# Kernel optimization log

Hardware: AMD Instinct MI355X
Metric: run time of the kernel (lower is better)

The kernel has to match this reference:

```python
import jax, jax.numpy as jnp
import numpy as np

B = 64          # number of scenes/graphs
OBJS = 2048     # objects per scene
N = B * OBJS    # total objects
D = 256         # representation_dim
K = 2           # num_channels


def setup_inputs() -> dict:
    key = jax.random.key(0)
    k1, k2, k3 = jax.random.split(key, 3)
    x_aggregation = jax.random.normal(k1, (N, D), dtype=jnp.float32)
    num_objs = jnp.full((B,), OBJS, dtype=jnp.int32)
    # glorot for att_shared [1, D]: fan_in + fan_out = 1 + D
    std_shared = float(np.sqrt(6.0 / (1 + D)))
    att_shared = jax.random.uniform(k2, (1, D), dtype=jnp.float32,
                                    minval=-std_shared, maxval=std_shared)
    # glorot for att_scale [K, 1]
    std_scale = float(np.sqrt(6.0 / (K + 1)))
    att_scale = jax.random.uniform(k3, (K, 1), dtype=jnp.float32,
                                   minval=-std_scale, maxval=std_scale)
    channel_bias = jnp.zeros((K, D), dtype=jnp.float32)
    return {"x_aggregation": x_aggregation, "num_objs": num_objs,
            "att_shared": att_shared, "att_scale": att_scale,
            "channel_bias": channel_bias}


def reference(x_aggregation, num_objs, att_shared, att_scale, channel_bias):
    batch_idx = jnp.repeat(jnp.arange(B), num_objs, total_repeat_length=N)  # [N]
    # scatter_mean: per-scene context features [B, D]
    seg_sum = jax.ops.segment_sum(x_aggregation, batch_idx, num_segments=B)
    counts = jnp.maximum(num_objs, 1).astype(x_aggregation.dtype)
    ctx = seg_sum / counts[:, None]
    attn_in = jax.nn.leaky_relu(x_aggregation + ctx[batch_idx], negative_slope=0.2)  # [N, D]
    # per-channel logits: ((attn_in + bias[k]) . att_shared) * scale[k]
    base = attn_in @ att_shared[0]                 # [N]
    bias_term = channel_bias @ att_shared[0]       # [K]
    logits = (base[:, None] + bias_term[None, :]) * att_scale[:, 0][None, :]  # [N, K]
    # per-channel segment softmax over objects within each scene
    m = jax.ops.segment_max(logits, batch_idx, num_segments=B)   # [B, K]
    z = jnp.exp(logits - m[batch_idx])
    s = jax.ops.segment_sum(z, batch_idx, num_segments=B)        # [B, K]
    attn_weights = z / s[batch_idx]                              # [N, K]
    # attention-weighted pooling per channel -> [B, D, K]
    weighted = x_aggregation[:, :, None] * attn_weights[:, None, :]  # [N, D, K]
    scene_features = jax.ops.segment_sum(weighted, batch_idx, num_segments=B)
    return scene_features, attn_weights
```

## Files before the change

kernel.cpp:

```cpp
#include <hip/hip_runtime.h>

#define B    64
#define OBJS 2048
#define NTOT (B * OBJS)
#define D    256
#define K    2
#define S1   16
#define CH   (OBJS / S1)
#define RPW  (CH / 4)

#define WS_P1  0
#define WS_UP  (1024 * 256)
#define WS_ZP  (WS_UP + 1024 * 512)
#define WS_E   (WS_ZP + 1024 * 8)

static __device__ __forceinline__ float lrelu02(float v) {
    return v > 0.0f ? v : 0.2f * v;
}

__global__ __launch_bounds__(256) void k1_partial(const float* __restrict__ x,
                                                  float* __restrict__ ws) {
    __shared__ float red[4 * D];
    int blk = blockIdx.x;
    int w = threadIdx.x >> 6, l = threadIdx.x & 63;
    int row0 = blk * CH + w * RPW;

    float4 acc = make_float4(0.f, 0.f, 0.f, 0.f);
    const float* px = x + (size_t)row0 * D + 4 * l;
#pragma unroll 8
    for (int j = 0; j < RPW; ++j) {
        float4 v = *(const float4*)(px + (size_t)j * D);
        acc.x += v.x; acc.y += v.y; acc.z += v.z; acc.w += v.w;
    }
    *(float4*)(red + w * D + 4 * l) = acc;
    __syncthreads();
    int t = threadIdx.x;
    if (t < 64) {
        float4 a = ((const float4*)(red        ))[t];
        float4 e = ((const float4*)(red +     D))[t];
        float4 f = ((const float4*)(red + 2 * D))[t];
        float4 g = ((const float4*)(red + 3 * D))[t];
        float4 s = make_float4(a.x + e.x + f.x + g.x, a.y + e.y + f.y + g.y,
                               a.z + e.z + f.z + g.z, a.w + e.w + f.w + g.w);
        *(float4*)(ws + WS_P1 + blk * D + 4 * t) = s;
    }
}

__global__ __launch_bounds__(256) void k2_main(const float* __restrict__ x,
                                               const int* __restrict__ num_objs,
                                               const float* __restrict__ att_scale,
                                               const float* __restrict__ att_shared,
                                               const float* __restrict__ channel_bias,
                                               float* __restrict__ ws) {
    __shared__ float sctx[D];
    __shared__ float sbt[2];
    __shared__ float ured[4 * D * K];
    int blk = blockIdx.x;
    int b = blk >> 4;
    int t = threadIdx.x;
    int w = t >> 6, l = t & 63;
    int row0 = blk * CH + w * RPW;

    {
        int cnt = num_objs[b]; if (cnt < 1) cnt = 1;
        float inv = 1.0f / (float)cnt;
        float s = 0.f;
#pragma unroll
        for (int c = 0; c < S1; ++c) s += ws[WS_P1 + (b * S1 + c) * D + t];
        sctx[t] = s * inv;
    }
    if (t < 64) {
        float4 a = ((const float4*)att_shared)[t];
#pragma unroll
        for (int k = 0; k < K; ++k) {
            float4 cb = ((const float4*)(channel_bias + k * D))[t];
            float v = a.x * cb.x + a.y * cb.y + a.z * cb.z + a.w * cb.w;
#pragma unroll
            for (int m = 32; m > 0; m >>= 1) v += __shfl_xor(v, m);
            if (t == 0) sbt[k] = v;
        }
    }
    __syncthreads();

    float4 a4 = ((const float4*)att_shared)[l];
    float4 ctx4 = *(const float4*)(sctx + 4 * l);
    float bt0 = sbt[0], bt1 = sbt[1];
    float s0 = att_scale[0], s1 = att_scale[1];

    float4 acc0 = make_float4(0.f, 0.f, 0.f, 0.f);
    float4 acc1 = make_float4(0.f, 0.f, 0.f, 0.f);
    float z0 = 0.f, z1 = 0.f;
    float my_e0 = 0.f, my_e1 = 0.f;
    int sel = l & 31;
    const float* px = x + (size_t)row0 * D + 4 * l;

#pragma unroll 4
    for (int j = 0; j < RPW; ++j) {
        float4 v = *(const float4*)(px + (size_t)j * D);
        float p = lrelu02(v.x + ctx4.x) * a4.x
                + lrelu02(v.y + ctx4.y) * a4.y
                + lrelu02(v.z + ctx4.z) * a4.z
                + lrelu02(v.w + ctx4.w) * a4.w;
#pragma unroll
        for (int m = 32; m > 0; m >>= 1) p += __shfl_xor(p, m);
        float e0 = __expf((p + bt0) * s0);
        float e1 = __expf((p + bt1) * s1);
        z0 += e0; z1 += e1;
        acc0.x += v.x * e0; acc0.y += v.y * e0; acc0.z += v.z * e0; acc0.w += v.w * e0;
        acc1.x += v.x * e1; acc1.y += v.y * e1; acc1.z += v.z * e1; acc1.w += v.w * e1;
        if (j == sel) { my_e0 = e0; my_e1 = e1; }
    }

    if (l < 32) ((float2*)(ws + WS_E))[row0 + l] = make_float2(my_e0, my_e1);
    if (l == 0) {
        ws[WS_ZP + blk * 8 + w * 2 + 0] = z0;
        ws[WS_ZP + blk * 8 + w * 2 + 1] = z1;
    }
    int base = w * (D * K) + l * 8;
    ured[base + 0] = acc0.x; ured[base + 1] = acc1.x;
    ured[base + 2] = acc0.y; ured[base + 3] = acc1.y;
    ured[base + 4] = acc0.z; ured[base + 5] = acc1.z;
    ured[base + 6] = acc0.w; ured[base + 7] = acc1.w;
    __syncthreads();
    if (t < 128) {
        float4 a = ((const float4*)(ured       ))[t];
        float4 e = ((const float4*)(ured +  512))[t];
        float4 f = ((const float4*)(ured + 1024))[t];
        float4 g = ((const float4*)(ured + 1536))[t];
        float4 s = make_float4(a.x + e.x + f.x + g.x, a.y + e.y + f.y + g.y,
                               a.z + e.z + f.z + g.z, a.w + e.w + f.w + g.w);
        *(float4*)(ws + WS_UP + blk * (D * K) + 4 * t) = s;
    }
}

__global__ __launch_bounds__(256) void k3_final(const float* __restrict__ ws,
                                                float* __restrict__ out) {
    __shared__ float zsh[2];
    int b = blockIdx.x;
    int t = threadIdx.x;
    int w = t >> 6, l = t & 63;

    if (w < 2) {
        float v = ws[WS_ZP + (b * S1 + (l >> 2)) * 8 + (l & 3) * 2 + w];
#pragma unroll
        for (int m = 32; m > 0; m >>= 1) v += __shfl_xor(v, m);
        if (l == 0) zsh[w] = v;
    }
    __syncthreads();
    float z0 = zsh[0], z1 = zsh[1];

#pragma unroll
    for (int j = t; j < D * K; j += 256) {
        float s = 0.f;
#pragma unroll
        for (int c = 0; c < S1; ++c) s += ws[WS_UP + (b * S1 + c) * (D * K) + j];
        out[b * (D * K) + j] = s / ((j & 1) ? z1 : z0);
    }
    const float2* E = (const float2*)(ws + WS_E);
    float2* W = (float2*)(out + B * D * K);
#pragma unroll
    for (int i = t; i < OBJS; i += 256) {
        float2 e = E[b * OBJS + i];
        W[b * OBJS + i] = make_float2(e.x / z0, e.y / z1);
    }
}

extern "C" void kernel_launch(void* const* d_in, const int* in_sizes, int n_in,
                              void* d_out, int out_size, void* d_ws, size_t ws_size,
                              hipStream_t stream) {
    const float* x            = (const float*)d_in[0];
    const int*   num_objs     = (const int*)d_in[1];
    const float* att_shared   = (const float*)d_in[2];
    const float* att_scale    = (const float*)d_in[3];
    const float* channel_bias = (const float*)d_in[4];
    float* ws  = (float*)d_ws;
    float* out = (float*)d_out;

    k1_partial<<<B * S1, 256, 0, stream>>>(x, ws);
    k2_main<<<B * S1, 256, 0, stream>>>(x, num_objs, att_scale, att_shared,
                                        channel_bias, ws);
    k3_final<<<B, 256, 0, stream>>>(ws, out);
}
```

Measured before the change: 222.8 us.

## Fuse three kernels into one with per-scene spin barriers and register-cached rows

Merges the segment-sum, attention-pooling and finalize kernels into one launch that keeps each block's rows in registers and LDS. Scene-local atomic barriers replace the kernel boundaries, so x is read from global memory once instead of twice and the stored unnormalized exponentials disappear. The fused kernel relies on all 512 blocks being co-resident; if they are not, the spin barriers deadlock until the timeout breaks them. It also raises register and LDS pressure.

```diff
diff --git a/kernel.cpp b/kernel.cpp
--- a/kernel.cpp
+++ b/kernel.cpp
@@ -5,70 +5,97 @@
 #define NTOT (B * OBJS)
 #define D    256
 #define K    2
-#define S1   16
-#define CH   (OBJS / S1)
-#define RPW  (CH / 4)
+
+#define SPB   8
+#define GRID  (B * SPB)
+#define RPB   (OBJS / SPB)
+#define RPWV  (RPB / 4)
+#define NREG  45
+#define NLDS  19
 
 #define WS_P1  0
-#define WS_UP  (1024 * 256)
-#define WS_ZP  (WS_UP + 1024 * 512)
-#define WS_E   (WS_ZP + 1024 * 8)
+#define WS_UP  (GRID * 4 * 256)
+#define WS_ZP  (WS_UP + GRID * 512)
+#define WS_CNT (WS_ZP + GRID * 2)
 
 static __device__ __forceinline__ float lrelu02(float v) {
     return v > 0.0f ? v : 0.2f * v;
 }
 
-__global__ __launch_bounds__(256) void k1_partial(const float* __restrict__ x,
-                                                  float* __restrict__ ws) {
-    __shared__ float red[4 * D];
-    int blk = blockIdx.x;
-    int w = threadIdx.x >> 6, l = threadIdx.x & 63;
-    int row0 = blk * CH + w * RPW;
-
-    float4 acc = make_float4(0.f, 0.f, 0.f, 0.f);
-    const float* px = x + (size_t)row0 * D + 4 * l;
-#pragma unroll 8
-    for (int j = 0; j < RPW; ++j) {
-        float4 v = *(const float4*)(px + (size_t)j * D);
-        acc.x += v.x; acc.y += v.y; acc.z += v.z; acc.w += v.w;
-    }
-    *(float4*)(red + w * D + 4 * l) = acc;
-    __syncthreads();
-    int t = threadIdx.x;
-    if (t < 64) {
-        float4 a = ((const float4*)(red        ))[t];
-        float4 e = ((const float4*)(red +     D))[t];
-        float4 f = ((const float4*)(red + 2 * D))[t];
-        float4 g = ((const float4*)(red + 3 * D))[t];
-        float4 s = make_float4(a.x + e.x + f.x + g.x, a.y + e.y + f.y + g.y,
-                               a.z + e.z + f.z + g.z, a.w + e.w + f.w + g.w);
-        *(float4*)(ws + WS_P1 + blk * D + 4 * t) = s;
-    }
-}
-
-__global__ __launch_bounds__(256) void k2_main(const float* __restrict__ x,
-                                               const int* __restrict__ num_objs,
-                                               const float* __restrict__ att_scale,
-                                               const float* __restrict__ att_shared,
-                                               const float* __restrict__ channel_bias,
-                                               float* __restrict__ ws) {
+static __device__ __forceinline__ float ldg_agent(const float* p) {
+    return __hip_atomic_load(p, __ATOMIC_RELAXED, __HIP_MEMORY_SCOPE_AGENT);
+}
+
+static __device__ __forceinline__ void scene_barrier(int* cnt, int expect) {
+    __builtin_amdgcn_fence(__ATOMIC_RELEASE, "agent");
+    __syncthreads();
+    if (threadIdx.x == 0) {
+        __hip_atomic_fetch_add(cnt, 1, __ATOMIC_ACQ_REL, __HIP_MEMORY_SCOPE_AGENT);
+        int it = 0;
+        while (__hip_atomic_load(cnt, __ATOMIC_ACQUIRE, __HIP_MEMORY_SCOPE_AGENT) < expect) {
+            __builtin_amdgcn_s_sleep(2);
+            if (++it > (1 << 26)) break;
+        }
+    }
+    __syncthreads();
+    __builtin_amdgcn_fence(__ATOMIC_ACQUIRE, "agent");
+}
+
+#define ROW_BODY(JCONST, V)                                                   \
+    {                                                                         \
+        float p = lrelu02((V).x + ctx4.x) * a4.x                              \
+                + lrelu02((V).y + ctx4.y) * a4.y                              \
+                + lrelu02((V).z + ctx4.z) * a4.z                              \
+                + lrelu02((V).w + ctx4.w) * a4.w;                             \
+        _Pragma("unroll")                                                     \
+        for (int m_ = 32; m_ > 0; m_ >>= 1) p += __shfl_xor(p, m_);           \
+        float e0_ = __expf((p + bt0) * s0);                                   \
+        float e1_ = __expf((p + bt1) * s1);                                   \
+        if ((JCONST) == l) { e0c = e0_; e1c = e1_; }                          \
+        acc0.x += (V).x * e0_; acc0.y += (V).y * e0_;                         \
+        acc0.z += (V).z * e0_; acc0.w += (V).w * e0_;                         \
+        acc1.x += (V).x * e1_; acc1.y += (V).y * e1_;                         \
+        acc1.z += (V).z * e1_; acc1.w += (V).w * e1_;                         \
+        z0 += e0_; z1 += e1_;                                                 \
+    }
+
+__global__ __launch_bounds__(256, 2)
+void fused_kernel(const float* __restrict__ x,
+                  const int* __restrict__ num_objs,
+                  const float* __restrict__ att_scale,
+                  const float* __restrict__ att_shared,
+                  const float* __restrict__ channel_bias,
+                  float* __restrict__ ws,
+                  float* __restrict__ out) {
+    __shared__ float xlds[4 * NLDS * D];
     __shared__ float sctx[D];
     __shared__ float sbt[2];
-    __shared__ float ured[4 * D * K];
+    __shared__ float zsh[8];
+
     int blk = blockIdx.x;
-    int b = blk >> 4;
+    int b = blk >> 3, c = blk & 7;
     int t = threadIdx.x;
     int w = t >> 6, l = t & 63;
-    int row0 = blk * CH + w * RPW;
-
-    {
-        int cnt = num_objs[b]; if (cnt < 1) cnt = 1;
-        float inv = 1.0f / (float)cnt;
-        float s = 0.f;
-#pragma unroll
-        for (int c = 0; c < S1; ++c) s += ws[WS_P1 + (b * S1 + c) * D + t];
-        sctx[t] = s * inv;
-    }
+    int* cnt1 = (int*)(ws + WS_CNT) + b;
+    int* cnt2 = (int*)(ws + WS_CNT) + 64 + b;
+
+    const float4* px = (const float4*)x + (size_t)(blk * RPB + w * RPWV) * (D / 4) + l;
+    float4 xr[NREG];
+    float4 csum = make_float4(0.f, 0.f, 0.f, 0.f);
+#pragma unroll
+    for (int j = 0; j < NREG; ++j) {
+        float4 v = px[(size_t)j * (D / 4)];
+        xr[j] = v;
+        csum.x += v.x; csum.y += v.y; csum.z += v.z; csum.w += v.w;
+    }
+#pragma unroll
+    for (int j = NREG; j < RPWV; ++j) {
+        float4 v = px[(size_t)j * (D / 4)];
+        csum.x += v.x; csum.y += v.y; csum.z += v.z; csum.w += v.w;
+        *(float4*)&xlds[(w * NLDS + (j - NREG)) * D + 4 * l] = v;
+    }
+    *(float4*)&ws[WS_P1 + (size_t)(blk * 4 + w) * D + 4 * l] = csum;
+
     if (t < 64) {
         float4 a = ((const float4*)att_shared)[t];
 #pragma unroll
@@ -80,9 +107,23 @@
             if (t == 0) sbt[k] = v;
         }
     }
-    __syncthreads();
-
-    float4 a4 = ((const float4*)att_shared)[l];
+
+    scene_barrier(cnt1, SPB);
+
+    {
+        int cntv = num_objs[b]; if (cntv < 1) cntv = 1;
+        float inv = 1.0f / (float)cntv;
+        float s = 0.f;
+#pragma unroll
+        for (int cc = 0; cc < SPB; ++cc)
+#pragma unroll
+            for (int ww = 0; ww < 4; ++ww)
+                s += ldg_agent(&ws[WS_P1 + (size_t)((b * SPB + cc) * 4 + ww) * D + t]);
+        sctx[t] = s * inv;
+    }
+    __syncthreads();
+
+    float4 a4   = ((const float4*)att_shared)[l];
     float4 ctx4 = *(const float4*)(sctx + 4 * l);
     float bt0 = sbt[0], bt1 = sbt[1];
     float s0 = att_scale[0], s1 = att_scale[1];
@@ -90,78 +131,65 @@
     float4 acc0 = make_float4(0.f, 0.f, 0.f, 0.f);
     float4 acc1 = make_float4(0.f, 0.f, 0.f, 0.f);
     float z0 = 0.f, z1 = 0.f;
-    float my_e0 = 0.f, my_e1 = 0.f;
-    int sel = l & 31;
-    const float* px = x + (size_t)row0 * D + 4 * l;
-
-#pragma unroll 4
-    for (int j = 0; j < RPW; ++j) {
-        float4 v = *(const float4*)(px + (size_t)j * D);
-        float p = lrelu02(v.x + ctx4.x) * a4.x
-                + lrelu02(v.y + ctx4.y) * a4.y
-                + lrelu02(v.z + ctx4.z) * a4.z
-                + lrelu02(v.w + ctx4.w) * a4.w;
-#pragma unroll
-        for (int m = 32; m > 0; m >>= 1) p += __shfl_xor(p, m);
-        float e0 = __expf((p + bt0) * s0);
-        float e1 = __expf((p + bt1) * s1);
-        z0 += e0; z1 += e1;
-        acc0.x += v.x * e0; acc0.y += v.y * e0; acc0.z += v.z * e0; acc0.w += v.w * e0;
-        acc1.x += v.x * e1; acc1.y += v.y * e1; acc1.z += v.z * e1; acc1.w += v.w * e1;
-        if (j == sel) { my_e0 = e0; my_e1 = e1; }
-    }
-
-    if (l < 32) ((float2*)(ws + WS_E))[row0 + l] = make_float2(my_e0, my_e1);
-    if (l == 0) {
-        ws[WS_ZP + blk * 8 + w * 2 + 0] = z0;
-        ws[WS_ZP + blk * 8 + w * 2 + 1] = z1;
-    }
-    int base = w * (D * K) + l * 8;
-    ured[base + 0] = acc0.x; ured[base + 1] = acc1.x;
-    ured[base + 2] = acc0.y; ured[base + 3] = acc1.y;
-    ured[base + 4] = acc0.z; ured[base + 5] = acc1.z;
-    ured[base + 6] = acc0.w; ured[base + 7] = acc1.w;
+    float e0c = 0.f, e1c = 0.f;
+
+#pragma unroll
+    for (int j = 0; j < NREG; ++j) ROW_BODY(j, xr[j]);
+#pragma unroll
+    for (int j = NREG; j < RPWV; ++j) {
+        float4 v = *(const float4*)&xlds[(w * NLDS + (j - NREG)) * D + 4 * l];
+        ROW_BODY(j, v);
+    }
+
+    __syncthreads();
+    if (l == 0) { zsh[w * 2] = z0; zsh[w * 2 + 1] = z1; }
+    {
+        int base = w * (D * K) + l * 8;
+        xlds[base + 0] = acc0.x; xlds[base + 1] = acc1.x;
+        xlds[base + 2] = acc0.y; xlds[base + 3] = acc1.y;
+        xlds[base + 4] = acc0.z; xlds[base + 5] = acc1.z;
+        xlds[base + 6] = acc0.w; xlds[base + 7] = acc1.w;
+    }
     __syncthreads();
     if (t < 128) {
-        float4 a = ((const float4*)(ured       ))[t];
-        float4 e = ((const float4*)(ured +  512))[t];
-        float4 f = ((const float4*)(ured + 1024))[t];
-        float4 g = ((const float4*)(ured + 1536))[t];
-        float4 s = make_float4(a.x + e.x + f.x + g.x, a.y + e.y + f.y + g.y,
-                               a.z + e.z + f.z + g.z, a.w + e.w + f.w + g.w);
-        *(float4*)(ws + WS_UP + blk * (D * K) + 4 * t) = s;
-    }
-}
-
-__global__ __launch_bounds__(256) void k3_final(const float* __restrict__ ws,
-                                                float* __restrict__ out) {
-    __shared__ float zsh[2];
-    int b = blockIdx.x;
-    int t = threadIdx.x;
-    int w = t >> 6, l = t & 63;
-
-    if (w < 2) {
-        float v = ws[WS_ZP + (b * S1 + (l >> 2)) * 8 + (l & 3) * 2 + w];
-#pragma unroll
-        for (int m = 32; m > 0; m >>= 1) v += __shfl_xor(v, m);
-        if (l == 0) zsh[w] = v;
-    }
-    __syncthreads();
-    float z0 = zsh[0], z1 = zsh[1];
-
-#pragma unroll
-    for (int j = t; j < D * K; j += 256) {
-        float s = 0.f;
-#pragma unroll
-        for (int c = 0; c < S1; ++c) s += ws[WS_UP + (b * S1 + c) * (D * K) + j];
-        out[b * (D * K) + j] = s / ((j & 1) ? z1 : z0);
-    }
-    const float2* E = (const float2*)(ws + WS_E);
-    float2* W = (float2*)(out + B * D * K);
-#pragma unroll
-    for (int i = t; i < OBJS; i += 256) {
-        float2 e = E[b * OBJS + i];
-        W[b * OBJS + i] = make_float2(e.x / z0, e.y / z1);
+        float4 a = ((const float4*)(xlds       ))[t];
+        float4 e = ((const float4*)(xlds +  512))[t];
+        float4 f = ((const float4*)(xlds + 1024))[t];
+        float4 g = ((const float4*)(xlds + 1536))[t];
+        float4 s4 = make_float4(a.x + e.x + f.x + g.x, a.y + e.y + f.y + g.y,
+                                a.z + e.z + f.z + g.z, a.w + e.w + f.w + g.w);
+        *(float4*)&ws[WS_UP + (size_t)blk * (D * K) + 4 * t] = s4;
+    }
+    if (t == 0) {
+        ws[WS_ZP + blk * 2 + 0] = zsh[0] + zsh[2] + zsh[4] + zsh[6];
+        ws[WS_ZP + blk * 2 + 1] = zsh[1] + zsh[3] + zsh[5] + zsh[7];
+    }
+
+    scene_barrier(cnt2, SPB);
+
+    float z0T = 0.f, z1T = 0.f;
+#pragma unroll
+    for (int cc = 0; cc < SPB; ++cc) {
+        z0T += ldg_agent(&ws[WS_ZP + (b * SPB + cc) * 2 + 0]);
+        z1T += ldg_agent(&ws[WS_ZP + (b * SPB + cc) * 2 + 1]);
+    }
+
+    {
+        float2* W = (float2*)(out + B * D * K);
+        int row = blk * RPB + w * RPWV + l;
+        W[row] = make_float2(e0c / z0T, e1c / z1T);
+    }
+
+    if (c == 0) {
+#pragma unroll
+        for (int rep = 0; rep < 2; ++rep) {
+            int j = t + rep * 256;
+            float s = 0.f;
+#pragma unroll
+            for (int cc = 0; cc < SPB; ++cc)
+                s += ldg_agent(&ws[WS_UP + (size_t)(b * SPB + cc) * (D * K) + j]);
+            out[b * (D * K) + j] = s / ((j & 1) ? z1T : z0T);
+        }
     }
 }
 
@@ -176,8 +204,9 @@
     float* ws  = (float*)d_ws;
     float* out = (float*)d_out;
 
-    k1_partial<<<B * S1, 256, 0, stream>>>(x, ws);
-    k2_main<<<B * S1, 256, 0, stream>>>(x, num_objs, att_scale, att_shared,
-                                        channel_bias, ws);
-    k3_final<<<B, 256, 0, stream>>>(ws, out);
-}
+    (void)hipMemsetAsync((char*)d_ws + (size_t)WS_CNT * sizeof(float), 0,
+                         128 * sizeof(int), stream);
+
+    fused_kernel<<<GRID, 256, 0, stream>>>(x, num_objs, att_scale, att_shared,
+                                           channel_bias, ws, out);
+}
```

After: 528.1 us. 2.37x slower.

## Batch per-row dot reductions through LDS transpose instead of per-row wave shuffles

Applied to the files above, without the earlier changes.

The main kernel now loads 8 rows at a time per wave. It writes per-lane partial dot products to a padded LDS tile and reduces them transposed, so one shuffle tree serves 8 rows instead of six shuffles per row. The exp weights are broadcast through LDS to apply the weighted accumulation. The final kernel replaces divisions with reciprocal multiplies and writes attention weights as float4. The trade-off is more LDS traffic and register pressure from holding 8 float4 rows, and there is no barrier between the LDS writes and reads within a wave (wave-synchronous assumption).

```diff
diff --git a/kernel.cpp b/kernel.cpp
--- a/kernel.cpp
+++ b/kernel.cpp
@@ -52,22 +52,25 @@
                                                const float* __restrict__ att_shared,
                                                const float* __restrict__ channel_bias,
                                                float* __restrict__ ws) {
+    __shared__ float pl[4 * 576];
+    __shared__ float esm[4 * 16];
     __shared__ float sctx[D];
     __shared__ float sbt[2];
-    __shared__ float ured[4 * D * K];
+
     int blk = blockIdx.x;
     int b = blk >> 4;
     int t = threadIdx.x;
     int w = t >> 6, l = t & 63;
+    int r = l & 7, s = l >> 3;
     int row0 = blk * CH + w * RPW;
 
     {
         int cnt = num_objs[b]; if (cnt < 1) cnt = 1;
         float inv = 1.0f / (float)cnt;
-        float s = 0.f;
-#pragma unroll
-        for (int c = 0; c < S1; ++c) s += ws[WS_P1 + (b * S1 + c) * D + t];
-        sctx[t] = s * inv;
+        float sum = 0.f;
+#pragma unroll
+        for (int c = 0; c < S1; ++c) sum += ws[WS_P1 + (b * S1 + c) * D + t];
+        sctx[t] = sum * inv;
     }
     if (t < 64) {
         float4 a = ((const float4*)att_shared)[t];
@@ -82,7 +85,7 @@
     }
     __syncthreads();
 
-    float4 a4 = ((const float4*)att_shared)[l];
+    float4 a4   = ((const float4*)att_shared)[l];
     float4 ctx4 = *(const float4*)(sctx + 4 * l);
     float bt0 = sbt[0], bt1 = sbt[1];
     float s0 = att_scale[0], s1 = att_scale[1];
@@ -90,46 +93,80 @@
     float4 acc0 = make_float4(0.f, 0.f, 0.f, 0.f);
     float4 acc1 = make_float4(0.f, 0.f, 0.f, 0.f);
     float z0 = 0.f, z1 = 0.f;
-    float my_e0 = 0.f, my_e1 = 0.f;
-    int sel = l & 31;
+    float e0c = 0.f, e1c = 0.f;
+    float* pw = pl  + w * 576;
+    float* ew = esm + w * 16;
     const float* px = x + (size_t)row0 * D + 4 * l;
 
-#pragma unroll 4
-    for (int j = 0; j < RPW; ++j) {
-        float4 v = *(const float4*)(px + (size_t)j * D);
-        float p = lrelu02(v.x + ctx4.x) * a4.x
-                + lrelu02(v.y + ctx4.y) * a4.y
-                + lrelu02(v.z + ctx4.z) * a4.z
-                + lrelu02(v.w + ctx4.w) * a4.w;
-#pragma unroll
-        for (int m = 32; m > 0; m >>= 1) p += __shfl_xor(p, m);
-        float e0 = __expf((p + bt0) * s0);
-        float e1 = __expf((p + bt1) * s1);
-        z0 += e0; z1 += e1;
-        acc0.x += v.x * e0; acc0.y += v.y * e0; acc0.z += v.z * e0; acc0.w += v.w * e0;
-        acc1.x += v.x * e1; acc1.y += v.y * e1; acc1.z += v.z * e1; acc1.w += v.w * e1;
-        if (j == sel) { my_e0 = e0; my_e1 = e1; }
-    }
-
-    if (l < 32) ((float2*)(ws + WS_E))[row0 + l] = make_float2(my_e0, my_e1);
+#pragma unroll
+    for (int g = 0; g < 4; ++g) {
+        float4 v0 = *(const float4*)(px + (size_t)(g * 8 + 0) * D);
+        float4 v1 = *(const float4*)(px + (size_t)(g * 8 + 1) * D);
+        float4 v2 = *(const float4*)(px + (size_t)(g * 8 + 2) * D);
+        float4 v3 = *(const float4*)(px + (size_t)(g * 8 + 3) * D);
+        float4 v4 = *(const float4*)(px + (size_t)(g * 8 + 4) * D);
+        float4 v5 = *(const float4*)(px + (size_t)(g * 8 + 5) * D);
+        float4 v6 = *(const float4*)(px + (size_t)(g * 8 + 6) * D);
+        float4 v7 = *(const float4*)(px + (size_t)(g * 8 + 7) * D);
+
+#define PDOT(V) (lrelu02((V).x + ctx4.x) * a4.x + lrelu02((V).y + ctx4.y) * a4.y \
+               + lrelu02((V).z + ctx4.z) * a4.z + lrelu02((V).w + ctx4.w) * a4.w)
+        pw[l * 9 + 0] = PDOT(v0); pw[l * 9 + 1] = PDOT(v1);
+        pw[l * 9 + 2] = PDOT(v2); pw[l * 9 + 3] = PDOT(v3);
+        pw[l * 9 + 4] = PDOT(v4); pw[l * 9 + 5] = PDOT(v5);
+        pw[l * 9 + 6] = PDOT(v6); pw[l * 9 + 7] = PDOT(v7);
+#undef PDOT
+        float tr = 0.f;
+#pragma unroll
+        for (int q = 0; q < 8; ++q) tr += pw[(s * 8 + q) * 9 + r];
+        tr += __shfl_xor(tr, 8);
+        tr += __shfl_xor(tr, 16);
+        tr += __shfl_xor(tr, 32);
+
+        float e0 = __expf((tr + bt0) * s0);
+        float e1 = __expf((tr + bt1) * s1);
+        if (((l >> 3) & 3) == g) { e0c = e0; e1c = e1; }
+        if (l < 8) { ew[2 * l] = e0; ew[2 * l + 1] = e1; }
+        float4 E0 = *(const float4*)(ew + 0);
+        float4 E1 = *(const float4*)(ew + 4);
+        float4 E2 = *(const float4*)(ew + 8);
+        float4 E3 = *(const float4*)(ew + 12);
+        z0 += E0.x + E0.z + E1.x + E1.z + E2.x + E2.z + E3.x + E3.z;
+        z1 += E0.y + E0.w + E1.y + E1.w + E2.y + E2.w + E3.y + E3.w;
+
+#define ACC(V, EA, EB) { acc0.x += (V).x * (EA); acc0.y += (V).y * (EA);      \
+                         acc0.z += (V).z * (EA); acc0.w += (V).w * (EA);      \
+                         acc1.x += (V).x * (EB); acc1.y += (V).y * (EB);      \
+                         acc1.z += (V).z * (EB); acc1.w += (V).w * (EB); }
+        ACC(v0, E0.x, E0.y) ACC(v1, E0.z, E0.w)
+        ACC(v2, E1.x, E1.y) ACC(v3, E1.z, E1.w)
+        ACC(v4, E2.x, E2.y) ACC(v5, E2.z, E2.w)
+        ACC(v6, E3.x, E3.y) ACC(v7, E3.z, E3.w)
+#undef ACC
+    }
+
+    if (l < 32) ((float2*)(ws + WS_E))[row0 + l] = make_float2(e0c, e1c);
     if (l == 0) {
         ws[WS_ZP + blk * 8 + w * 2 + 0] = z0;
         ws[WS_ZP + blk * 8 + w * 2 + 1] = z1;
     }
-    int base = w * (D * K) + l * 8;
-    ured[base + 0] = acc0.x; ured[base + 1] = acc1.x;
-    ured[base + 2] = acc0.y; ured[base + 3] = acc1.y;
-    ured[base + 4] = acc0.z; ured[base + 5] = acc1.z;
-    ured[base + 6] = acc0.w; ured[base + 7] = acc1.w;
+    __syncthreads();
+    {
+        int base = w * (D * K) + l * 8;
+        pl[base + 0] = acc0.x; pl[base + 1] = acc1.x;
+        pl[base + 2] = acc0.y; pl[base + 3] = acc1.y;
+        pl[base + 4] = acc0.z; pl[base + 5] = acc1.z;
+        pl[base + 6] = acc0.w; pl[base + 7] = acc1.w;
+    }
     __syncthreads();
     if (t < 128) {
-        float4 a = ((const float4*)(ured       ))[t];
-        float4 e = ((const float4*)(ured +  512))[t];
-        float4 f = ((const float4*)(ured + 1024))[t];
-        float4 g = ((const float4*)(ured + 1536))[t];
-        float4 s = make_float4(a.x + e.x + f.x + g.x, a.y + e.y + f.y + g.y,
-                               a.z + e.z + f.z + g.z, a.w + e.w + f.w + g.w);
-        *(float4*)(ws + WS_UP + blk * (D * K) + 4 * t) = s;
+        float4 a = ((const float4*)(pl       ))[t];
+        float4 e = ((const float4*)(pl +  512))[t];
+        float4 f = ((const float4*)(pl + 1024))[t];
+        float4 g = ((const float4*)(pl + 1536))[t];
+        float4 s4 = make_float4(a.x + e.x + f.x + g.x, a.y + e.y + f.y + g.y,
+                                a.z + e.z + f.z + g.z, a.w + e.w + f.w + g.w);
+        *(float4*)(ws + WS_UP + (size_t)blk * (D * K) + 4 * t) = s4;
     }
 }
 
@@ -148,20 +185,21 @@
     }
     __syncthreads();
     float z0 = zsh[0], z1 = zsh[1];
+    float iz0 = 1.0f / z0, iz1 = 1.0f / z1;
 
 #pragma unroll
     for (int j = t; j < D * K; j += 256) {
         float s = 0.f;
 #pragma unroll
         for (int c = 0; c < S1; ++c) s += ws[WS_UP + (b * S1 + c) * (D * K) + j];
-        out[b * (D * K) + j] = s / ((j & 1) ? z1 : z0);
-    }
-    const float2* E = (const float2*)(ws + WS_E);
-    float2* W = (float2*)(out + B * D * K);
-#pragma unroll
-    for (int i = t; i < OBJS; i += 256) {
-        float2 e = E[b * OBJS + i];
-        W[b * OBJS + i] = make_float2(e.x / z0, e.y / z1);
+        out[b * (D * K) + j] = s * ((j & 1) ? iz1 : iz0);
+    }
+    const float4* E = (const float4*)(ws + WS_E);
+    float4* W = (float4*)(out + B * D * K);
+#pragma unroll
+    for (int i = t; i < OBJS / 2; i += 256) {
+        float4 e = E[b * (OBJS / 2) + i];
+        W[b * (OBJS / 2) + i] = make_float4(e.x * iz0, e.y * iz1, e.z * iz0, e.w * iz1);
     }
 }
 
```

Measured after the change: 222.7 us. No clear change (-0.1%).
